# Performance work log

Measured on AMD Instinct MI355X. Metric: run time of the kernel, lower is better.

Reference implementation:

```python
import jax, jax.numpy as jnp
import numpy as np
import math

B, S, D, H = 1, 4096, 1024, 16
HD = D // H  # head_dim = 64


def setup_inputs() -> dict:
    key = jax.random.key(0)
    ks = jax.random.split(key, 6)
    x = jax.random.normal(ks[0], (B, S, D), dtype=jnp.float32)
    # Llama-style rotary frequencies: theta = 10000^{-2i/head_dim}
    inv_freq = 1.0 / (10000.0 ** (jnp.arange(0, HD, 2, dtype=jnp.float32) / HD))  # (HD/2,)
    t = jnp.arange(S, dtype=jnp.float32)
    freqs = jnp.outer(t, inv_freq)  # (S, HD/2)
    cos = jnp.cos(freqs)
    sin = jnp.sin(freqs)
    # additive causal mask (S, S): 0 on/below diagonal, -inf above
    mask = jnp.where(jnp.tril(jnp.ones((S, S), dtype=bool)), 0.0, -jnp.inf).astype(jnp.float32)
    scale = 1.0 / math.sqrt(D)
    wq = jax.random.normal(ks[1], (D, D), dtype=jnp.float32) * scale
    wk = jax.random.normal(ks[2], (D, D), dtype=jnp.float32) * scale
    wv = jax.random.normal(ks[3], (D, D), dtype=jnp.float32) * scale
    wo = jax.random.normal(ks[4], (D, D), dtype=jnp.float32) * scale
    return {"x": x, "cos": cos, "sin": sin, "mask": mask,
            "wq": wq, "wk": wk, "wv": wv, "wo": wo, "start_pos": 0}


def _rope(t, cos, sin):
    # t: (b, s, h, hd); cos/sin: (s, hd/2). Interleaved-pair complex rotation.
    b, s, h, hd = t.shape
    tr = t.reshape(b, s, h, hd // 2, 2)
    te, to = tr[..., 0], tr[..., 1]
    c = cos[None, :, None, :]
    sn = sin[None, :, None, :]
    oe = te * c - to * sn
    oo = te * sn + to * c
    return jnp.stack([oe, oo], axis=-1).reshape(b, s, h, hd)


def reference(x, cos, sin, mask, wq, wk, wv, wo, start_pos):
    b, s, d = x.shape
    h, hd = H, HD
    # Linear layers: y = x @ W.T (torch nn.Linear convention, W is (out,in))
    xq = (x @ wq.T).reshape(b, s, h, hd)
    xk = (x @ wk.T).reshape(b, s, h, hd)
    xv = (x @ wv.T).reshape(b, s, h, hd)
    xq = _rope(xq, cos, sin)
    xk = _rope(xk, cos, sin)
    # (b, h, s, hd)
    xq = xq.transpose(0, 2, 1, 3)
    xk = xk.transpose(0, 2, 1, 3)
    xv = xv.transpose(0, 2, 1, 3)
    scores = jnp.einsum('bhqd,bhkd->bhqk', xq, xk) / math.sqrt(hd)
    scores = scores + mask[None, None, :, :]
    attn = jax.nn.softmax(scores.astype(jnp.float32), axis=-1).astype(xq.dtype)
    out = jnp.einsum('bhqk,bhkd->bhqd', attn, xv)
    out = out.transpose(0, 2, 1, 3).reshape(b, s, d)
    return out @ wo.T
```

## Files before the change

### kernel.cpp

```cpp
#include <hip/hip_runtime.h>
#include <hip/hip_bf16.h>
#include <math.h>

typedef __bf16 bf16;
typedef __bf16 bf16x4 __attribute__((ext_vector_type(4)));
typedef __bf16 bf16x8 __attribute__((ext_vector_type(8)));
typedef float floatx4 __attribute__((ext_vector_type(4)));
typedef short short4v __attribute__((ext_vector_type(4)));

#define S_LEN 4096
#define DM 1024
#define NH 16
#define HD 64

#define GM 4096
#define GN 1024
#define GK 1024
#define FST 68

#define QSCALE 0.18033688011112042f

#define GLDS16(gp, lp) __builtin_amdgcn_global_load_lds( \
    (const __attribute__((address_space(1))) void*)(gp), \
    (__attribute__((address_space(3))) void*)(lp), 16, 0, 0)

__global__ void cvt_bf16(const float* __restrict__ x,  const float* __restrict__ wq,
                         const float* __restrict__ wk, const float* __restrict__ wv,
                         const float* __restrict__ wo, bf16* __restrict__ dst)
{
    size_t i4 = ((size_t)blockIdx.x * 256 + threadIdx.x) * 4;
    const float* src; size_t off;
    const size_t M1 = (size_t)1 << 20;
    if      (i4 < 4 * M1) { src = x;  off = i4;          }
    else if (i4 < 5 * M1) { src = wq; off = i4 - 4 * M1; }
    else if (i4 < 6 * M1) { src = wk; off = i4 - 5 * M1; }
    else if (i4 < 7 * M1) { src = wv; off = i4 - 6 * M1; }
    else                  { src = wo; off = i4 - 7 * M1; }
    float4 v = *(const float4*)(src + off);
    bf16x4 o = { (bf16)v.x, (bf16)v.y, (bf16)v.z, (bf16)v.w };
    *(bf16x4*)(&dst[i4]) = o;
}

__launch_bounds__(256)
__global__ void gemm_qkv(const bf16* __restrict__ A,
                         const bf16* __restrict__ B0, const bf16* __restrict__ B1,
                         const bf16* __restrict__ B2,
                         const float* __restrict__ cosp, const float* __restrict__ sinp,
                         bf16* __restrict__ Qw, bf16* __restrict__ Kw,
                         bf16* __restrict__ VTw)
{
    const int bz = blockIdx.z;
    const bf16* __restrict__ B = (bz == 0) ? B0 : (bz == 1 ? B1 : B2);

    const int tid  = threadIdx.x;
    const int wave = tid >> 6;
    const int lane = tid & 63;
    const int wm   = (wave >> 1) * 32;
    const int wn   = (wave & 1) * 64;
    const int lrow = lane >> 4;
    const int lcol = lane & 15;

    const int m0 = blockIdx.y * 64;
    const int n0 = blockIdx.x * 128;

    __shared__ __align__(16) bf16 As[2][64 * 64];
    __shared__ __align__(16) bf16 Bs[2][128 * 64];

    floatx4 acc[2][4];
    #pragma unroll
    for (int i = 0; i < 2; i++)
        #pragma unroll
        for (int j = 0; j < 4; j++) acc[i][j] = (floatx4){0.f, 0.f, 0.f, 0.f};

    const int swc = (((lane & 7) ^ ((lane >> 3) & 7))) * 8;
    const bf16* ga0 = A + (size_t)(m0 + wave * 16 + (lane >> 3)) * GK + swc;
    const bf16* gb0 = B + (size_t)(n0 + wave * 32 + (lane >> 3)) * GK + swc;
    const int kof0 = ((0 + lrow) ^ (lcol & 7)) * 8;
    const int kof1 = ((4 + lrow) ^ (lcol & 7)) * 8;

    #pragma unroll
    for (int i = 0; i < 2; i++)
        GLDS16(ga0 + (size_t)i * 8 * GK, &As[0][(wave * 16 + i * 8) * 64]);
    #pragma unroll
    for (int i = 0; i < 4; i++)
        GLDS16(gb0 + (size_t)i * 8 * GK, &Bs[0][(wave * 32 + i * 8) * 64]);
    __syncthreads();

    int cur = 0;
    for (int kt = 0; kt < GK; kt += 64) {
        if (kt + 64 < GK) {
            #pragma unroll
            for (int i = 0; i < 2; i++)
                GLDS16(ga0 + kt + 64 + (size_t)i * 8 * GK, &As[cur ^ 1][(wave * 16 + i * 8) * 64]);
            #pragma unroll
            for (int i = 0; i < 4; i++)
                GLDS16(gb0 + kt + 64 + (size_t)i * 8 * GK, &Bs[cur ^ 1][(wave * 32 + i * 8) * 64]);
        }
        #pragma unroll
        for (int ks = 0; ks < 2; ks++) {
            const int ko = ks ? kof1 : kof0;
            bf16x8 af[2], bfr[4];
            #pragma unroll
            for (int t = 0; t < 2; t++)
                af[t]  = *(const bf16x8*)(&As[cur][(wm + t * 16 + lcol) * 64 + ko]);
            #pragma unroll
            for (int t = 0; t < 4; t++)
                bfr[t] = *(const bf16x8*)(&Bs[cur][(wn + t * 16 + lcol) * 64 + ko]);
            #pragma unroll
            for (int mt = 0; mt < 2; mt++)
                #pragma unroll
                for (int nt = 0; nt < 4; nt++)
                    acc[mt][nt] = __builtin_amdgcn_mfma_f32_16x16x32_bf16(af[mt], bfr[nt], acc[mt][nt], 0, 0, 0);
        }
        __syncthreads();
        cur ^= 1;
    }

    if (bz < 2) {
        bf16* __restrict__ C = bz ? Kw : Qw;
        const float qs = (bz == 0) ? QSCALE : 1.0f;
        const bool odd = (lcol & 1);
        #pragma unroll
        for (int mt = 0; mt < 2; mt++)
            #pragma unroll
            for (int nt = 0; nt < 4; nt++) {
                int i = (nt * 16 + lcol) >> 1;
                #pragma unroll
                for (int r = 0; r < 4; r++) {
                    float v  = acc[mt][nt][r];
                    float pv = __shfl_xor(v, 1, 64);
                    int s = m0 + wm + mt * 16 + lrow * 4 + r;
                    float c  = cosp[s * 32 + i];
                    float sn = sinp[s * 32 + i];
                    float ov = odd ? (pv * sn + v * c) : (v * c - pv * sn);
                    C[(size_t)s * GN + n0 + wn + nt * 16 + lcol] = (bf16)(ov * qs);
                }
            }
    } else {
        #pragma unroll
        for (int mt = 0; mt < 2; mt++)
            #pragma unroll
            for (int nt = 0; nt < 4; nt++) {
                int col = n0 + wn + nt * 16 + lcol;
                int s   = m0 + wm + mt * 16 + lrow * 4;
                bf16x4 ov = { (bf16)acc[mt][nt][0], (bf16)acc[mt][nt][1],
                              (bf16)acc[mt][nt][2], (bf16)acc[mt][nt][3] };
                *(bf16x4*)(&VTw[(size_t)col * S_LEN + s]) = ov;
            }
    }
}

__launch_bounds__(256, 4)
__global__ void flash_attn(const bf16* __restrict__ Q, const bf16* __restrict__ K,
                           const bf16* __restrict__ VT,
                           float* __restrict__ O0, float* __restrict__ O1,
                           float* __restrict__ L0, float* __restrict__ L1)
{
    const int pi   = blockIdx.x >> 1;
    const int p    = blockIdx.x & 1;
    const int h    = blockIdx.y;
    const int tid  = threadIdx.x;
    const int wave = tid >> 6;
    const int lane = tid & 63;
    const int lrow = lane >> 4;
    const int lcol = lane & 15;

    const int qtA = pi;
    const int qtB = 63 - pi;

    float* __restrict__ Op = p ? O1 : O0;
    float* __restrict__ Lp = p ? L1 : L0;

    __shared__ __align__(16) bf16 Ks[2][64 * FST];
    __shared__ __align__(16) bf16 Vs[2][64 * FST];

    const int q0A = qtA * 64 + wave * 16;
    const int q0B = qtB * 64 + wave * 16;

    const bf16* qpA = Q + (size_t)(q0A + lcol) * DM + h * HD;
    const bf16* qpB = Q + (size_t)(q0B + lcol) * DM + h * HD;
    bf16x8 qfA[2], qfB[2];
    qfA[0] = *(const bf16x8*)(qpA + 0 + lrow * 8);
    qfA[1] = *(const bf16x8*)(qpA + 32 + lrow * 8);
    qfB[0] = *(const bf16x8*)(qpB + 0 + lrow * 8);
    qfB[1] = *(const bf16x8*)(qpB + 32 + lrow * 8);

    float lA = 0.f, lB = 0.f;
    floatx4 oaccA[4], oaccB[4];
    #pragma unroll
    for (int nt = 0; nt < 4; nt++) {
        oaccA[nt] = (floatx4){0.f, 0.f, 0.f, 0.f};
        oaccB[nt] = (floatx4){0.f, 0.f, 0.f, 0.f};
    }

    const int  srow = tid >> 3;
    const int  sch  = (tid & 7) * 8;
    const bf16* kp  = K  + (size_t)srow * DM + h * HD + sch;
    const bf16* vp  = VT + (size_t)(h * HD + srow) * S_LEN + sch;
    const int  wof  = srow * FST + sch;

    {
        size_t ko = (size_t)p * 64 * DM;
        size_t vo = (size_t)p * 64;
        uint4 a = *(const uint4*)(kp + ko);
        uint4 b = *(const uint4*)(kp + ko + (size_t)32 * DM);
        uint4 c = *(const uint4*)(vp + vo);
        uint4 d = *(const uint4*)(vp + vo + (size_t)32 * S_LEN);
        *(uint4*)(&Ks[0][wof])            = a;
        *(uint4*)(&Ks[0][wof + 32 * FST]) = b;
        *(uint4*)(&Vs[0][wof])            = c;
        *(uint4*)(&Vs[0][wof + 32 * FST]) = d;
    }
    __syncthreads();

    uint4 kr0, kr1, vr0, vr1;
    for (int t = p; t <= qtB; t += 2) {
        const int  cur  = ((t - p) >> 1) & 1;
        const bool more = (t + 2 <= qtB);
        const bool actA = (t <= qtA);

        if (more) {
            size_t ko = (size_t)(t + 2) * 64 * DM;
            size_t vo = (size_t)(t + 2) * 64;
            kr0 = *(const uint4*)(kp + ko);
            kr1 = *(const uint4*)(kp + ko + (size_t)32 * DM);
            vr0 = *(const uint4*)(vp + vo);
            vr1 = *(const uint4*)(vp + vo + (size_t)32 * S_LEN);
        }

        short4v pbA[4], pbB[4];
        const bool diagA = (t == qtA);
        const bool diagB = (t == qtB);
        #pragma unroll
        for (int nt = 0; nt < 4; nt++) {
            floatx4 zB = (floatx4){0.f, 0.f, 0.f, 0.f};
            floatx4 zA = (floatx4){0.f, 0.f, 0.f, 0.f};
            #pragma unroll
            for (int ks = 0; ks < 2; ks++) {
                bf16x8 kf = *(const bf16x8*)(&Ks[cur][(nt * 16 + lcol) * FST + ks * 32 + lrow * 8]);
                zB = __builtin_amdgcn_mfma_f32_16x16x32_bf16(kf, qfB[ks], zB, 0, 0, 0);
                if (actA)
                    zA = __builtin_amdgcn_mfma_f32_16x16x32_bf16(kf, qfA[ks], zA, 0, 0, 0);
            }
            if (diagB) {
                #pragma unroll
                for (int r = 0; r < 4; r++) {
                    int kg = t * 64 + nt * 16 + lrow * 4 + r;
                    float pr = exp2f(zB[r]);
                    if (kg > q0B + lcol) pr = 0.f;
                    zB[r] = pr; lB += pr;
                }
            } else {
                #pragma unroll
                for (int r = 0; r < 4; r++) {
                    float pr = exp2f(zB[r]);
                    zB[r] = pr; lB += pr;
                }
            }
            bf16x4 pvB = { (bf16)zB[0], (bf16)zB[1], (bf16)zB[2], (bf16)zB[3] };
            pbB[nt] = __builtin_bit_cast(short4v, pvB);
            if (actA) {
                if (diagA) {
                    #pragma unroll
                    for (int r = 0; r < 4; r++) {
                        int kg = t * 64 + nt * 16 + lrow * 4 + r;
                        float pr = exp2f(zA[r]);
                        if (kg > q0A + lcol) pr = 0.f;
                        zA[r] = pr; lA += pr;
                    }
                } else {
                    #pragma unroll
                    for (int r = 0; r < 4; r++) {
                        float pr = exp2f(zA[r]);
                        zA[r] = pr; lA += pr;
                    }
                }
                bf16x4 pvA = { (bf16)zA[0], (bf16)zA[1], (bf16)zA[2], (bf16)zA[3] };
                pbA[nt] = __builtin_bit_cast(short4v, pvA);
            }
        }

        #pragma unroll
        for (int nt = 0; nt < 4; nt++)
            #pragma unroll
            for (int kt = 0; kt < 4; kt++) {
                bf16x4 va = *(const bf16x4*)(&Vs[cur][(nt * 16 + lcol) * FST + kt * 16 + lrow * 4]);
                short4v vas = __builtin_bit_cast(short4v, va);
                oaccB[nt] = __builtin_amdgcn_mfma_f32_16x16x16bf16_1k(vas, pbB[kt], oaccB[nt], 0, 0, 0);
                if (actA)
                    oaccA[nt] = __builtin_amdgcn_mfma_f32_16x16x16bf16_1k(vas, pbA[kt], oaccA[nt], 0, 0, 0);
            }

        if (more) {
            int nxt = cur ^ 1;
            *(uint4*)(&Ks[nxt][wof])            = kr0;
            *(uint4*)(&Ks[nxt][wof + 32 * FST]) = kr1;
            *(uint4*)(&Vs[nxt][wof])            = vr0;
            *(uint4*)(&Vs[nxt][wof + 32 * FST]) = vr1;
        }
        __syncthreads();
    }

    lA += __shfl_xor(lA, 16, 64);
    lA += __shfl_xor(lA, 32, 64);
    lB += __shfl_xor(lB, 16, 64);
    lB += __shfl_xor(lB, 32, 64);
    if (lrow == 0) {
        Lp[h * S_LEN + q0A + lcol] = lA;
        Lp[h * S_LEN + q0B + lcol] = lB;
    }
    #pragma unroll
    for (int nt = 0; nt < 4; nt++) {
        *(floatx4*)(&Op[(size_t)(q0A + lcol) * DM + h * HD + nt * 16 + lrow * 4]) = oaccA[nt];
        *(floatx4*)(&Op[(size_t)(q0B + lcol) * DM + h * HD + nt * 16 + lrow * 4]) = oaccB[nt];
    }
}

__global__ void combine_kernel(const float* __restrict__ O0, const float* __restrict__ O1,
                               const float* __restrict__ L0, const float* __restrict__ L1,
                               bf16* __restrict__ Aw)
{
    int i4 = (blockIdx.x * 256 + threadIdx.x) * 4;
    int q = i4 >> 10;
    int c = i4 & 1023;
    int h = c >> 6;
    float rl = 1.f / (L0[h * S_LEN + q] + L1[h * S_LEN + q]);
    float4 a = *(const float4*)(O0 + i4);
    float4 b = *(const float4*)(O1 + i4);
    bf16x4 o = { (bf16)((a.x + b.x) * rl), (bf16)((a.y + b.y) * rl),
                 (bf16)((a.z + b.z) * rl), (bf16)((a.w + b.w) * rl) };
    *(bf16x4*)(&Aw[i4]) = o;
}

__launch_bounds__(256)
__global__ void gemm_out(const bf16* __restrict__ A, const bf16* __restrict__ B,
                         float* __restrict__ out)
{
    const int tid  = threadIdx.x;
    const int wave = tid >> 6;
    const int lane = tid & 63;
    const int wm   = (wave >> 1) * 32;
    const int wn   = (wave & 1) * 64;
    const int lrow = lane >> 4;
    const int lcol = lane & 15;

    const int m0 = blockIdx.y * 64;
    const int n0 = blockIdx.x * 128;

    __shared__ __align__(16) bf16 As[2][64 * 64];
    __shared__ __align__(16) bf16 Bs[2][128 * 64];

    floatx4 acc[2][4];
    #pragma unroll
    for (int i = 0; i < 2; i++)
        #pragma unroll
        for (int j = 0; j < 4; j++) acc[i][j] = (floatx4){0.f, 0.f, 0.f, 0.f};

    const int swc = (((lane & 7) ^ ((lane >> 3) & 7))) * 8;
    const bf16* ga0 = A + (size_t)(m0 + wave * 16 + (lane >> 3)) * GK + swc;
    const bf16* gb0 = B + (size_t)(n0 + wave * 32 + (lane >> 3)) * GK + swc;
    const int kof0 = ((0 + lrow) ^ (lcol & 7)) * 8;
    const int kof1 = ((4 + lrow) ^ (lcol & 7)) * 8;

    #pragma unroll
    for (int i = 0; i < 2; i++)
        GLDS16(ga0 + (size_t)i * 8 * GK, &As[0][(wave * 16 + i * 8) * 64]);
    #pragma unroll
    for (int i = 0; i < 4; i++)
        GLDS16(gb0 + (size_t)i * 8 * GK, &Bs[0][(wave * 32 + i * 8) * 64]);
    __syncthreads();

    int cur = 0;
    for (int kt = 0; kt < GK; kt += 64) {
        if (kt + 64 < GK) {
            #pragma unroll
            for (int i = 0; i < 2; i++)
                GLDS16(ga0 + kt + 64 + (size_t)i * 8 * GK, &As[cur ^ 1][(wave * 16 + i * 8) * 64]);
            #pragma unroll
            for (int i = 0; i < 4; i++)
                GLDS16(gb0 + kt + 64 + (size_t)i * 8 * GK, &Bs[cur ^ 1][(wave * 32 + i * 8) * 64]);
        }
        #pragma unroll
        for (int ks = 0; ks < 2; ks++) {
            const int ko = ks ? kof1 : kof0;
            bf16x8 af[2], bfr[4];
            #pragma unroll
            for (int t = 0; t < 2; t++)
                af[t]  = *(const bf16x8*)(&As[cur][(wm + t * 16 + lcol) * 64 + ko]);
            #pragma unroll
            for (int t = 0; t < 4; t++)
                bfr[t] = *(const bf16x8*)(&Bs[cur][(wn + t * 16 + lcol) * 64 + ko]);
            #pragma unroll
            for (int mt = 0; mt < 2; mt++)
                #pragma unroll
                for (int nt = 0; nt < 4; nt++)
                    acc[mt][nt] = __builtin_amdgcn_mfma_f32_16x16x32_bf16(af[mt], bfr[nt], acc[mt][nt], 0, 0, 0);
        }
        __syncthreads();
        cur ^= 1;
    }

    #pragma unroll
    for (int mt = 0; mt < 2; mt++)
        #pragma unroll
        for (int nt = 0; nt < 4; nt++)
            #pragma unroll
            for (int r = 0; r < 4; r++) {
                int row = m0 + wm + mt * 16 + lrow * 4 + r;
                int col = n0 + wn + nt * 16 + lcol;
                out[(size_t)row * GN + col] = acc[mt][nt][r];
            }
}

extern "C" void kernel_launch(void* const* d_in, const int* in_sizes, int n_in,
                              void* d_out, int out_size, void* d_ws, size_t ws_size,
                              hipStream_t stream) {
    const float* x    = (const float*)d_in[0];
    const float* cosp = (const float*)d_in[1];
    const float* sinp = (const float*)d_in[2];
    const float* wq   = (const float*)d_in[4];
    const float* wk   = (const float*)d_in[5];
    const float* wv   = (const float*)d_in[6];
    const float* wo   = (const float*)d_in[7];
    float* out = (float*)d_out;

    const size_t SD = (size_t)S_LEN * DM;
    const size_t DD = (size_t)DM * DM;
    bf16* xb  = (bf16*)d_ws;
    bf16* wqb = xb + SD;
    bf16* wkb = wqb + DD;
    bf16* wvb = wkb + DD;
    bf16* wob = wvb + DD;
    bf16* Qw  = wob + DD;
    bf16* Kw  = Qw + SD;
    bf16* VTw = Kw + SD;
    bf16* Aw  = VTw + SD;
    float* O0f = (float*)(Aw + SD);
    float* O1f = O0f + SD;
    float* L0f = O1f + SD;
    float* L1f = L0f + (size_t)S_LEN * NH;

    cvt_bf16<<<8192, 256, 0, stream>>>(x, wq, wk, wv, wo, xb);
    gemm_qkv<<<dim3(GN / 128, GM / 64, 3), 256, 0, stream>>>(
        xb, wqb, wkb, wvb, cosp, sinp, Qw, Kw, VTw);
    flash_attn<<<dim3(64, NH), 256, 0, stream>>>(Qw, Kw, VTw, O0f, O1f, L0f, L1f);
    combine_kernel<<<S_LEN * DM / 1024, 256, 0, stream>>>(O0f, O1f, L0f, L1f, Aw);
    gemm_out<<<dim3(GN / 128, GM / 64), 256, 0, stream>>>(Aw, wob, out);
}
```

Measured before the change: 284.2 us.

## Split attention KV range into fixed chunks instead of paired query tiles

The flash attention kernel no longer pairs a short and a long query tile per block, each processed with parity-split KV halves. Each block now handles one query tile over a chunk of up to 22 KV tiles, giving 126 blocks per head and up to three partial outputs. The combine kernel sums one to three partials depending on the query tile. The goal is simpler per-block code, fewer registers, and more blocks, at the cost of a third partial buffer, more combine traffic, and uneven chunk lengths.

Result: no change. 287.1 us (+1.0%).

```diff
diff --git a/kernel.cpp b/kernel.cpp
--- a/kernel.cpp
+++ b/kernel.cpp
@@ -17,6 +17,9 @@
 #define GN 1024
 #define GK 1024
 #define FST 68
+
+#define CHK 22
+#define FBLK 126
 
 #define QSCALE 0.18033688011112042f
 
@@ -154,10 +157,15 @@
 __global__ void flash_attn(const bf16* __restrict__ Q, const bf16* __restrict__ K,
                            const bf16* __restrict__ VT,
                            float* __restrict__ O0, float* __restrict__ O1,
-                           float* __restrict__ L0, float* __restrict__ L1)
+                           float* __restrict__ O2,
+                           float* __restrict__ L0, float* __restrict__ L1,
+                           float* __restrict__ L2)
 {
-    const int pi   = blockIdx.x >> 1;
-    const int p    = blockIdx.x & 1;
+    const int b = blockIdx.x;
+    int qi, c;
+    if (b < 22)      { qi = b; c = 0; }
+    else if (b < 66) { int i = b - 22; qi = 22 + (i >> 1); c = i & 1; }
+    else             { int i = b - 66; int g = i / 3; qi = 44 + g; c = i - g * 3; }
     const int h    = blockIdx.y;
     const int tid  = threadIdx.x;
     const int wave = tid >> 6;
@@ -165,33 +173,27 @@
     const int lrow = lane >> 4;
     const int lcol = lane & 15;
 
-    const int qtA = pi;
-    const int qtB = 63 - pi;
-
-    float* __restrict__ Op = p ? O1 : O0;
-    float* __restrict__ Lp = p ? L1 : L0;
+    const int t0   = c * CHK;
+    const int tmax = t0 + CHK - 1;
+    const int tend = (tmax < qi) ? tmax : qi;
+
+    float* __restrict__ Op = (c == 0) ? O0 : (c == 1 ? O1 : O2);
+    float* __restrict__ Lp = (c == 0) ? L0 : (c == 1 ? L1 : L2);
 
     __shared__ __align__(16) bf16 Ks[2][64 * FST];
     __shared__ __align__(16) bf16 Vs[2][64 * FST];
 
-    const int q0A = qtA * 64 + wave * 16;
-    const int q0B = qtB * 64 + wave * 16;
-
-    const bf16* qpA = Q + (size_t)(q0A + lcol) * DM + h * HD;
-    const bf16* qpB = Q + (size_t)(q0B + lcol) * DM + h * HD;
-    bf16x8 qfA[2], qfB[2];
-    qfA[0] = *(const bf16x8*)(qpA + 0 + lrow * 8);
-    qfA[1] = *(const bf16x8*)(qpA + 32 + lrow * 8);
-    qfB[0] = *(const bf16x8*)(qpB + 0 + lrow * 8);
-    qfB[1] = *(const bf16x8*)(qpB + 32 + lrow * 8);
-
-    float lA = 0.f, lB = 0.f;
-    floatx4 oaccA[4], oaccB[4];
-    #pragma unroll
-    for (int nt = 0; nt < 4; nt++) {
-        oaccA[nt] = (floatx4){0.f, 0.f, 0.f, 0.f};
-        oaccB[nt] = (floatx4){0.f, 0.f, 0.f, 0.f};
-    }
+    const int q0 = qi * 64 + wave * 16;
+
+    const bf16* qp = Q + (size_t)(q0 + lcol) * DM + h * HD;
+    bf16x8 qf[2];
+    qf[0] = *(const bf16x8*)(qp + 0 + lrow * 8);
+    qf[1] = *(const bf16x8*)(qp + 32 + lrow * 8);
+
+    float l = 0.f;
+    floatx4 oacc[4];
+    #pragma unroll
+    for (int nt = 0; nt < 4; nt++) oacc[nt] = (floatx4){0.f, 0.f, 0.f, 0.f};
 
     const int  srow = tid >> 3;
     const int  sch  = (tid & 7) * 8;
@@ -200,84 +202,60 @@
     const int  wof  = srow * FST + sch;
 
     {
-        size_t ko = (size_t)p * 64 * DM;
-        size_t vo = (size_t)p * 64;
+        size_t ko = (size_t)t0 * 64 * DM;
+        size_t vo = (size_t)t0 * 64;
         uint4 a = *(const uint4*)(kp + ko);
-        uint4 b = *(const uint4*)(kp + ko + (size_t)32 * DM);
-        uint4 c = *(const uint4*)(vp + vo);
+        uint4 bb = *(const uint4*)(kp + ko + (size_t)32 * DM);
+        uint4 cc = *(const uint4*)(vp + vo);
         uint4 d = *(const uint4*)(vp + vo + (size_t)32 * S_LEN);
         *(uint4*)(&Ks[0][wof])            = a;
-        *(uint4*)(&Ks[0][wof + 32 * FST]) = b;
-        *(uint4*)(&Vs[0][wof])            = c;
+        *(uint4*)(&Ks[0][wof + 32 * FST]) = bb;
+        *(uint4*)(&Vs[0][wof])            = cc;
         *(uint4*)(&Vs[0][wof + 32 * FST]) = d;
     }
     __syncthreads();
 
     uint4 kr0, kr1, vr0, vr1;
-    for (int t = p; t <= qtB; t += 2) {
-        const int  cur  = ((t - p) >> 1) & 1;
-        const bool more = (t + 2 <= qtB);
-        const bool actA = (t <= qtA);
+    for (int t = t0; t <= tend; ++t) {
+        const int  cur  = (t - t0) & 1;
+        const bool more = (t + 1 <= tend);
 
         if (more) {
-            size_t ko = (size_t)(t + 2) * 64 * DM;
-            size_t vo = (size_t)(t + 2) * 64;
+            size_t ko = (size_t)(t + 1) * 64 * DM;
+            size_t vo = (size_t)(t + 1) * 64;
             kr0 = *(const uint4*)(kp + ko);
             kr1 = *(const uint4*)(kp + ko + (size_t)32 * DM);
             vr0 = *(const uint4*)(vp + vo);
             vr1 = *(const uint4*)(vp + vo + (size_t)32 * S_LEN);
         }
 
-        short4v pbA[4], pbB[4];
-        const bool diagA = (t == qtA);
-        const bool diagB = (t == qtB);
+        short4v pb[4];
+        const bool diag = (t == qi);
         #pragma unroll
         for (int nt = 0; nt < 4; nt++) {
-            floatx4 zB = (floatx4){0.f, 0.f, 0.f, 0.f};
-            floatx4 zA = (floatx4){0.f, 0.f, 0.f, 0.f};
+            floatx4 z = (floatx4){0.f, 0.f, 0.f, 0.f};
             #pragma unroll
             for (int ks = 0; ks < 2; ks++) {
                 bf16x8 kf = *(const bf16x8*)(&Ks[cur][(nt * 16 + lcol) * FST + ks * 32 + lrow * 8]);
-                zB = __builtin_amdgcn_mfma_f32_16x16x32_bf16(kf, qfB[ks], zB, 0, 0, 0);
-                if (actA)
-                    zA = __builtin_amdgcn_mfma_f32_16x16x32_bf16(kf, qfA[ks], zA, 0, 0, 0);
-            }
-            if (diagB) {
+                z = __builtin_amdgcn_mfma_f32_16x16x32_bf16(kf, qf[ks], z, 0, 0, 0);
+            }
+            if (diag) {
                 #pragma unroll
                 for (int r = 0; r < 4; r++) {
                     int kg = t * 64 + nt * 16 + lrow * 4 + r;
-                    float pr = exp2f(zB[r]);
-                    if (kg > q0B + lcol) pr = 0.f;
-                    zB[r] = pr; lB += pr;
+                    float pr = exp2f(z[r]);
+                    if (kg > q0 + lcol) pr = 0.f;
+                    z[r] = pr; l += pr;
                 }
             } else {
                 #pragma unroll
                 for (int r = 0; r < 4; r++) {
-                    float pr = exp2f(zB[r]);
-                    zB[r] = pr; lB += pr;
+                    float pr = exp2f(z[r]);
+                    z[r] = pr; l += pr;
                 }
             }
-            bf16x4 pvB = { (bf16)zB[0], (bf16)zB[1], (bf16)zB[2], (bf16)zB[3] };
-            pbB[nt] = __builtin_bit_cast(short4v, pvB);
-            if (actA) {
-                if (diagA) {
-                    #pragma unroll
-                    for (int r = 0; r < 4; r++) {
-                        int kg = t * 64 + nt * 16 + lrow * 4 + r;
-                        float pr = exp2f(zA[r]);
-                        if (kg > q0A + lcol) pr = 0.f;
-                        zA[r] = pr; lA += pr;
-                    }
-                } else {
-                    #pragma unroll
-                    for (int r = 0; r < 4; r++) {
-                        float pr = exp2f(zA[r]);
-                        zA[r] = pr; lA += pr;
-                    }
-                }
-                bf16x4 pvA = { (bf16)zA[0], (bf16)zA[1], (bf16)zA[2], (bf16)zA[3] };
-                pbA[nt] = __builtin_bit_cast(short4v, pvA);
-            }
+            bf16x4 pv = { (bf16)z[0], (bf16)z[1], (bf16)z[2], (bf16)z[3] };
+            pb[nt] = __builtin_bit_cast(short4v, pv);
         }
 
         #pragma unroll
@@ -286,9 +264,7 @@
             for (int kt = 0; kt < 4; kt++) {
                 bf16x4 va = *(const bf16x4*)(&Vs[cur][(nt * 16 + lcol) * FST + kt * 16 + lrow * 4]);
                 short4v vas = __builtin_bit_cast(short4v, va);
-                oaccB[nt] = __builtin_amdgcn_mfma_f32_16x16x16bf16_1k(vas, pbB[kt], oaccB[nt], 0, 0, 0);
-                if (actA)
-                    oaccA[nt] = __builtin_amdgcn_mfma_f32_16x16x16bf16_1k(vas, pbA[kt], oaccA[nt], 0, 0, 0);
+                oacc[nt] = __builtin_amdgcn_mfma_f32_16x16x16bf16_1k(vas, pb[kt], oacc[nt], 0, 0, 0);
             }
 
         if (more) {
@@ -301,34 +277,42 @@
         __syncthreads();
     }
 
-    lA += __shfl_xor(lA, 16, 64);
-    lA += __shfl_xor(lA, 32, 64);
-    lB += __shfl_xor(lB, 16, 64);
-    lB += __shfl_xor(lB, 32, 64);
-    if (lrow == 0) {
-        Lp[h * S_LEN + q0A + lcol] = lA;
-        Lp[h * S_LEN + q0B + lcol] = lB;
-    }
-    #pragma unroll
-    for (int nt = 0; nt < 4; nt++) {
-        *(floatx4*)(&Op[(size_t)(q0A + lcol) * DM + h * HD + nt * 16 + lrow * 4]) = oaccA[nt];
-        *(floatx4*)(&Op[(size_t)(q0B + lcol) * DM + h * HD + nt * 16 + lrow * 4]) = oaccB[nt];
-    }
-}
-
-__global__ void combine_kernel(const float* __restrict__ O0, const float* __restrict__ O1,
-                               const float* __restrict__ L0, const float* __restrict__ L1,
-                               bf16* __restrict__ Aw)
+    l += __shfl_xor(l, 16, 64);
+    l += __shfl_xor(l, 32, 64);
+    if (lrow == 0)
+        Lp[h * S_LEN + q0 + lcol] = l;
+    #pragma unroll
+    for (int nt = 0; nt < 4; nt++)
+        *(floatx4*)(&Op[(size_t)(q0 + lcol) * DM + h * HD + nt * 16 + lrow * 4]) = oacc[nt];
+}
+
+__global__ void combine3u(const float* __restrict__ O0, const float* __restrict__ O1,
+                          const float* __restrict__ O2,
+                          const float* __restrict__ L0, const float* __restrict__ L1,
+                          const float* __restrict__ L2,
+                          bf16* __restrict__ Aw)
 {
     int i4 = (blockIdx.x * 256 + threadIdx.x) * 4;
     int q = i4 >> 10;
-    int c = i4 & 1023;
-    int h = c >> 6;
-    float rl = 1.f / (L0[h * S_LEN + q] + L1[h * S_LEN + q]);
+    int cc = i4 & 1023;
+    int h = cc >> 6;
+    int qi = q >> 6;
+    int nc = qi / CHK + 1;
+    float l = L0[h * S_LEN + q];
     float4 a = *(const float4*)(O0 + i4);
-    float4 b = *(const float4*)(O1 + i4);
-    bf16x4 o = { (bf16)((a.x + b.x) * rl), (bf16)((a.y + b.y) * rl),
-                 (bf16)((a.z + b.z) * rl), (bf16)((a.w + b.w) * rl) };
+    float ox = a.x, oy = a.y, oz = a.z, ow = a.w;
+    if (nc > 1) {
+        l += L1[h * S_LEN + q];
+        float4 bq = *(const float4*)(O1 + i4);
+        ox += bq.x; oy += bq.y; oz += bq.z; ow += bq.w;
+    }
+    if (nc > 2) {
+        l += L2[h * S_LEN + q];
+        float4 cq = *(const float4*)(O2 + i4);
+        ox += cq.x; oy += cq.y; oz += cq.z; ow += cq.w;
+    }
+    float rl = 1.f / l;
+    bf16x4 o = { (bf16)(ox * rl), (bf16)(oy * rl), (bf16)(oz * rl), (bf16)(ow * rl) };
     *(bf16x4*)(&Aw[i4]) = o;
 }
 
@@ -439,11 +423,15 @@
     float* O1f = O0f + SD;
     float* L0f = O1f + SD;
     float* L1f = L0f + (size_t)S_LEN * NH;
+    float* O2f = L1f + (size_t)S_LEN * NH;
+    float* L2f = O2f + SD;
 
     cvt_bf16<<<8192, 256, 0, stream>>>(x, wq, wk, wv, wo, xb);
     gemm_qkv<<<dim3(GN / 128, GM / 64, 3), 256, 0, stream>>>(
         xb, wqb, wkb, wvb, cosp, sinp, Qw, Kw, VTw);
-    flash_attn<<<dim3(64, NH), 256, 0, stream>>>(Qw, Kw, VTw, O0f, O1f, L0f, L1f);
-    combine_kernel<<<S_LEN * DM / 1024, 256, 0, stream>>>(O0f, O1f, L0f, L1f, Aw);
+    flash_attn<<<dim3(FBLK, NH), 256, 0, stream>>>(
+        Qw, Kw, VTw, O0f, O1f, O2f, L0f, L1f, L2f);
+    combine3u<<<S_LEN * DM / 1024, 256, 0, stream>>>(
+        O0f, O1f, O2f, L0f, L1f, L2f, Aw);
     gemm_out<<<dim3(GN / 128, GM / 64), 256, 0, stream>>>(Aw, wob, out);
 }
```
